# Kernel tuning notes

Hardware: AMD Instinct MI355X
Metric: run time of the kernel (lower is better)

The kernel has to match this reference:

```python
import jax, jax.numpy as jnp
import numpy as np

N_E = 8192
E_DIM = 256
N_TOK = 32768
MU = 0.25  # commitment weight; beta=0 so diversity loss is skipped


def setup_inputs() -> dict:
    key = jax.random.key(0)
    k1, k2, k3 = jax.random.split(key, 3)
    x = jax.random.normal(k1, (N_TOK, E_DIM), dtype=jnp.float32)
    # codebook init: uniform(-1/n_e, 1/n_e) as in the torch module
    emb = jax.random.uniform(k2, (N_E, E_DIM), dtype=jnp.float32,
                             minval=-1.0 / N_E, maxval=1.0 / N_E)
    label = jax.random.randint(k3, (N_TOK,), 0, 10, dtype=jnp.int32)
    return {"x": x, "emb": emb, "label": label, "idx": 0}


def reference(x, emb, label, idx):
    # latent: [N, e_dim]
    latent = x.reshape(-1, emb.shape[1])
    # pairwise squared distances via norm + matmul: [N, n_e]
    d = (jnp.sum(latent * latent, axis=1, keepdims=True)
         + jnp.sum(emb * emb, axis=1)[None, :]
         - 2.0 * (latent @ emb.T))
    indices = jnp.argmin(d, axis=-1)                 # [N]
    x_q = emb[indices].reshape(x.shape)              # gather
    commitment_loss = jnp.mean(jnp.square(jax.lax.stop_gradient(x_q) - x))
    codebook_loss = jnp.mean(jnp.square(x_q - jax.lax.stop_gradient(x)))
    loss = codebook_loss + MU * commitment_loss      # beta=0 -> no diversity term
    x_q_out = x + jax.lax.stop_gradient(x_q - x)     # straight-through estimator
    return x_q_out, loss, indices.reshape(x.shape[:-1])
```

## Files before the change

kernel.cpp:

```cpp
#include <hip/hip_runtime.h>
#include <float.h>
#include <stdint.h>

#define N_TOK 32768
#define N_E   8192
#define EDIM  256
#define MU_W  0.25f
#define NSPLIT 4
#define NRANGE 2048
#define BMr 128
#define BNr 256
#define NT8 8
#define TQ  4
#define MARGIN_F 4096.0f
#define OFFSETF (-0x1p21f)
#define XSCALE 512.0f
#define ESCALE -131072.0f

typedef _Float16 f16;
typedef _Float16 f16x8 __attribute__((ext_vector_type(8)));
typedef _Float16 f16x4 __attribute__((ext_vector_type(4)));
typedef float f32x4 __attribute__((ext_vector_type(4)));
typedef unsigned int u32;
typedef unsigned long long u64;

#define WS_EMB16   0
#define WS_SX      4194304
#define WS_SE      4325376
#define WS_SE25    4358144
#define WS_CAND    4390912
#define WS_PART    6488064
#define WS_RCNT    6619136
#define WS_RLIST   6619392
#define WS_RBEST   6750464

__device__ inline void gload_lds16(const void* g, void* l) {
  __builtin_amdgcn_global_load_lds(
      (const __attribute__((address_space(1))) unsigned int*)g,
      (__attribute__((address_space(3))) unsigned int*)l, 16, 0, 0);
}

__device__ inline u32 umax_(u32 a, u32 b) { return a > b ? a : b; }
__device__ inline u32 umin_(u32 a, u32 b) { return a < b ? a : b; }

__device__ inline u32 med3u(u32 a, u32 b, u32 c) {
  u32 r;
  asm("v_med3_u32 %0, %1, %2, %3" : "=v"(r) : "v"(a), "v"(b), "v"(c));
  return r;
}

__device__ inline void ins4max(u32 v, u32& a, u32& b, u32& c, u32& d) {
  u32 na = umax_(a, v);
  u32 nb = med3u(a, b, v);
  u32 nc = med3u(b, c, v);
  u32 nd = med3u(c, d, v);
  a = na; b = nb; c = nc; d = nd;
}

__global__ void zero_kernel(u32* p) { p[0] = 0u; }

__global__ __launch_bounds__(256) void conv_kernel(const float* __restrict__ src,
                                                   char* __restrict__ dst16,
                                                   float* __restrict__ norms,
                                                   float* __restrict__ norms25,
                                                   float scale, int write16, int nrows) {
  int wave = threadIdx.x >> 6;
  int lane = threadIdx.x & 63;
  int row = blockIdx.x * 4 + wave;
  if (row >= nrows) return;
  const float4 v = *(const float4*)(src + (size_t)row * EDIM + lane * 4);
  float s = (v.x * v.x + v.y * v.y) + (v.z * v.z + v.w * v.w);
#pragma unroll
  for (int off = 32; off >= 1; off >>= 1) s += __shfl_xor(s, off);
  if (lane == 0) {
    norms[row] = s;
    if (norms25) norms25[row] = s * 0x1p25f;
  }
  if (write16) {
    f16x4 h;
    h[0] = (f16)(v.x * scale); h[1] = (f16)(v.y * scale);
    h[2] = (f16)(v.z * scale); h[3] = (f16)(v.w * scale);
    int sw = (row & 7) << 4;
    *(f16x4*)(dst16 + (size_t)row * 512 + ((lane * 8) ^ sw)) = h;
  }
}

__global__ __launch_bounds__(512, 2) void vq_main(const float* __restrict__ x,
                                                  const char* __restrict__ e16,
                                                  const float* __restrict__ se25,
                                                  u32* __restrict__ cand) {
  __shared__ __align__(16) char Abuf[128 * 512];
  __shared__ __align__(16) char Bbuf[2][256 * 128];
  __shared__ u32 scratch[8][4][16][4];

  const int tid = threadIdx.x;
  const int lane = tid & 63;
  const int wid = tid >> 6;
  const int wm = wid >> 2;
  const int wn = wid & 3;
  const int l15 = lane & 15;
  const int lg  = lane >> 4;
  const int split = blockIdx.x & 3;
  const int bm = (blockIdx.x >> 2) * BMr;
  const int nbase = split * NRANGE;

  {
    const int row = tid >> 2, seg = tid & 3;
    const float4* xs = (const float4*)(x + (size_t)(bm + row) * EDIM + seg * 64);
    const int sw = (row & 7) << 4;
    char* ab = Abuf + row * 512;
#pragma unroll
    for (int u = 0; u < 8; ++u) {
      float4 a0 = xs[2 * u], a1 = xs[2 * u + 1];
      f16x8 hv;
      hv[0] = (f16)(a0.x * XSCALE); hv[1] = (f16)(a0.y * XSCALE);
      hv[2] = (f16)(a0.z * XSCALE); hv[3] = (f16)(a0.w * XSCALE);
      hv[4] = (f16)(a1.x * XSCALE); hv[5] = (f16)(a1.y * XSCALE);
      hv[6] = (f16)(a1.z * XSCALE); hv[7] = (f16)(a1.w * XSCALE);
      *(f16x8*)(ab + ((seg * 128 + u * 16) ^ sw)) = hv;
    }
  }
  {
    const char* src = e16 + (size_t)nbase * 512;
#pragma unroll
    for (int j = 0; j < 4; ++j) {
      int tt = j * 512 + tid;
      gload_lds16(src + (size_t)(tt >> 3) * 512 + (tt & 7) * 16, Bbuf[0] + tt * 16);
    }
  }
  __syncthreads();

  u32 d1[16], d2[16], d3[16], d4[16];
#pragma unroll
  for (int s = 0; s < 16; ++s) { d1[s] = 0u; d2[s] = 0u; d3[s] = 0u; d4[s] = 0u; }

  int cur = 0;
  for (int t = 0; t < NT8; ++t) {
    float sev[4];
#pragma unroll
    for (int ni = 0; ni < 4; ++ni)
      sev[ni] = se25[nbase + t * 256 + wn * 64 + ni * 16 + l15] + OFFSETF;

    f32x4 acc[4][4];
#pragma unroll
    for (int mi = 0; mi < 4; ++mi)
#pragma unroll
      for (int ni = 0; ni < 4; ++ni)
        acc[mi][ni] = (f32x4){sev[ni], sev[ni], sev[ni], sev[ni]};

    for (int q = 0; q < TQ; ++q) {
      const int step = t * TQ + q;
      if (step + 1 < NT8 * TQ) {
        const int t2 = (step + 1) >> 2, q2 = (step + 1) & 3;
        const char* src = e16 + (size_t)(nbase + t2 * 256) * 512 + q2 * 128;
        char* dst = Bbuf[cur ^ 1];
#pragma unroll
        for (int j = 0; j < 4; ++j) {
          int tt = j * 512 + tid;
          gload_lds16(src + (size_t)(tt >> 3) * 512 + (tt & 7) * 16, dst + tt * 16);
        }
      }
#pragma unroll
      for (int kk = 0; kk < 2; ++kk) {
        f16x8 av[4], bv[4];
#pragma unroll
        for (int mi = 0; mi < 4; ++mi) {
          const int ar = wm * 64 + mi * 16 + l15;
          av[mi] = *(const f16x8*)(Abuf + ar * 512 +
                                   ((q * 128 + kk * 64 + lg * 16) ^ ((ar & 7) << 4)));
        }
#pragma unroll
        for (int ni = 0; ni < 4; ++ni) {
          const int br = wn * 64 + ni * 16 + l15;
          bv[ni] = *(const f16x8*)(Bbuf[cur] + br * 128 +
                                   ((kk * 64 + lg * 16) ^ ((br & 7) << 4)));
        }
#pragma unroll
        for (int mi = 0; mi < 4; ++mi)
#pragma unroll
          for (int ni = 0; ni < 4; ++ni)
            acc[mi][ni] = __builtin_amdgcn_mfma_f32_16x16x32_f16(av[mi], bv[ni], acc[mi][ni], 0, 0, 0);
      }
      if (q == TQ - 1) {
#pragma unroll
        for (int ni = 0; ni < 4; ++ni) {
          const u32 id = (u32)((t << 8) | (wn << 6) | (ni << 4) | l15);
#pragma unroll
          for (int mi = 0; mi < 4; ++mi)
#pragma unroll
            for (int r = 0; r < 4; ++r) {
              u32 up = (__float_as_uint(acc[mi][ni][r]) & 0xFFFFF800u) | id;
              int s = mi * 4 + r;
              ins4max(up, d1[s], d2[s], d3[s], d4[s]);
            }
        }
      }
      __syncthreads();
      cur ^= 1;
    }
  }

#pragma unroll
  for (int off = 8; off >= 1; off >>= 1) {
#pragma unroll
    for (int s = 0; s < 16; ++s) {
      u32 e1 = (u32)__shfl_xor((int)d1[s], off);
      u32 e2 = (u32)__shfl_xor((int)d2[s], off);
      u32 e3 = (u32)__shfl_xor((int)d3[s], off);
      u32 e4 = (u32)__shfl_xor((int)d4[s], off);
      ins4max(e1, d1[s], d2[s], d3[s], d4[s]);
      ins4max(e2, d1[s], d2[s], d3[s], d4[s]);
      ins4max(e3, d1[s], d2[s], d3[s], d4[s]);
      ins4max(e4, d1[s], d2[s], d3[s], d4[s]);
    }
  }
  if (l15 == 0) {
#pragma unroll
    for (int s = 0; s < 16; ++s) {
      scratch[wid][lg][s][0] = d1[s];
      scratch[wid][lg][s][1] = d2[s];
      scratch[wid][lg][s][2] = d3[s];
      scratch[wid][lg][s][3] = d4[s];
    }
  }
  __syncthreads();
  if (tid < 128) {
    const int row = tid;
    const int wmr = row >> 6, mi = (row >> 4) & 3, lgr = (row >> 2) & 3, rr = row & 3;
    const int s = mi * 4 + rr;
    u32 a1 = scratch[wmr * 4][lgr][s][0];
    u32 a2 = scratch[wmr * 4][lgr][s][1];
    u32 a3 = scratch[wmr * 4][lgr][s][2];
    u32 a4 = scratch[wmr * 4][lgr][s][3];
#pragma unroll
    for (int w = 1; w < 4; ++w) {
#pragma unroll
      for (int c = 0; c < 4; ++c)
        ins4max(scratch[wmr * 4 + w][lgr][s][c], a1, a2, a3, a4);
    }
    size_t base = (size_t)split * (N_TOK * 4) + (size_t)(bm + row) * 4;
    cand[base + 0] = a1; cand[base + 1] = a2; cand[base + 2] = a3; cand[base + 3] = a4;
  }
}

__global__ __launch_bounds__(256) void vq_gather_kernel(
    const float* __restrict__ x, const float* __restrict__ emb,
    const float* __restrict__ sx, const float* __restrict__ se,
    const u32* __restrict__ cand,
    float* __restrict__ out_q, float* __restrict__ out_idx,
    float* __restrict__ partials,
    u32* __restrict__ rcnt, u32* __restrict__ rlist, u64* __restrict__ rbest) {
  const int token = blockIdx.x;
  const int tid = threadIdx.x;
  __shared__ int s_j;
  __shared__ int s_cnt;
  __shared__ int s_cj[16];
  __shared__ float s_dv[16];
  __shared__ float red[4];

  if (tid == 0) {
    u32 u[16];
    float uf[16];
    float gmin = FLT_MAX;
#pragma unroll
    for (int sp = 0; sp < 4; ++sp)
#pragma unroll
      for (int c = 0; c < 4; ++c) {
        u32 v = cand[(size_t)sp * (N_TOK * 4) + (size_t)token * 4 + c];
        u[sp * 4 + c] = v;
        float f = __uint_as_float(v);
        uf[sp * 4 + c] = f;
        gmin = fminf(gmin, f);
      }
    bool guard = false;
#pragma unroll
    for (int sp = 0; sp < 4; ++sp) guard = guard || (uf[sp * 4 + 3] <= gmin + MARGIN_F);
    int cnt;
    if (guard) {
      u32 slot = atomicAdd(rcnt, 1u);
      rlist[slot] = (u32)token;
      rbest[slot] = ~0ull;
      cnt = -1;
    } else {
      cnt = 0;
#pragma unroll
      for (int sp = 0; sp < 4; ++sp)
#pragma unroll
        for (int c = 0; c < 4; ++c) {
          int k = sp * 4 + c;
          if (uf[k] <= gmin + MARGIN_F)
            s_cj[cnt++] = sp * NRANGE + (int)(u[k] & 0x7FFu);
        }
      if (cnt == 1) s_j = s_cj[0];
    }
    s_cnt = cnt;
  }
  __syncthreads();
  int cnt = s_cnt;
  if (cnt < 0) return;
  if (cnt > 1 && tid < cnt) {
    int j = s_cj[tid];
    const float* xr = x + (size_t)token * EDIM;
    const float* er = emb + (size_t)j * EDIM;
    float a = 0.f;
    for (int k = 0; k < EDIM; ++k) a = fmaf(xr[k], er[k], a);
    s_dv[tid] = (sx[token] + se[j]) - 2.0f * a;
  }
  __syncthreads();
  if (cnt > 1 && tid == 0) {
    float bd = s_dv[0]; int bj = s_cj[0];
    for (int c = 1; c < cnt; ++c) {
      float d = s_dv[c]; int j = s_cj[c];
      if (d < bd || (d == bd && j < bj)) { bd = d; bj = j; }
    }
    s_j = bj;
  }
  __syncthreads();
  const int j = s_j;
  if (tid == 0) out_idx[token] = (float)j;
  float xv = x[(size_t)token * EDIM + tid];
  float q  = emb[(size_t)j * EDIM + tid];
  float diff = q - xv;
  out_q[(size_t)token * EDIM + tid] = xv + diff;
  float sq = diff * diff;
#pragma unroll
  for (int off = 32; off >= 1; off >>= 1) sq += __shfl_xor(sq, off);
  const int wave = tid >> 6, lane = tid & 63;
  if (lane == 0) red[wave] = sq;
  __syncthreads();
  if (tid == 0) partials[token] = (red[0] + red[1]) + (red[2] + red[3]);
}

__global__ __launch_bounds__(256) void vq_rescan_scan(
    const float* __restrict__ x, const float* __restrict__ emb,
    const float* __restrict__ sx, const float* __restrict__ se,
    const u32* __restrict__ rcnt, const u32* __restrict__ rlist,
    u64* __restrict__ rbest) {
  const int tid = threadIdx.x;
  const int n = (int)rcnt[0];
  const int total = n * 32;
  __shared__ float xs[EDIM];
  __shared__ u64 rw[4];

  for (int w = blockIdx.x; w < total; w += gridDim.x) {
    const int it = w >> 5, chunk = w & 31;
    const int token = (int)rlist[it];
    __syncthreads();
    xs[tid] = x[(size_t)token * EDIM + tid];
    __syncthreads();
    const float sxt = sx[token];
    const int j = chunk * 256 + tid;
    const float* er = emb + (size_t)j * EDIM;
    float a = 0.f;
#pragma unroll 8
    for (int k4 = 0; k4 < 64; ++k4) {
      float4 e4 = ((const float4*)er)[k4];
      float4 x4 = ((const float4*)xs)[k4];
      a = fmaf(x4.x, e4.x, a);
      a = fmaf(x4.y, e4.y, a);
      a = fmaf(x4.z, e4.z, a);
      a = fmaf(x4.w, e4.w, a);
    }
    float d = (sxt + se[j]) - 2.0f * a;
    u64 pk = ((u64)__float_as_uint(d) << 32) | (u32)j;
    const int lane = tid & 63, wave = tid >> 6;
#pragma unroll
    for (int off = 32; off >= 1; off >>= 1) {
      u64 o = __shfl_xor(pk, off);
      pk = o < pk ? o : pk;
    }
    if (lane == 0) rw[wave] = pk;
    __syncthreads();
    if (tid == 0) {
      u64 b = rw[0];
#pragma unroll
      for (int ww = 1; ww < 4; ++ww) b = rw[ww] < b ? rw[ww] : b;
      atomicMin(rbest + it, b);
    }
  }
}

__global__ __launch_bounds__(256) void vq_rescan_write(
    const float* __restrict__ x, const float* __restrict__ emb,
    const u32* __restrict__ rcnt, const u32* __restrict__ rlist,
    const u64* __restrict__ rbest,
    float* __restrict__ out_q, float* __restrict__ out_idx,
    float* __restrict__ partials) {
  const int tid = threadIdx.x;
  const int n = (int)rcnt[0];
  __shared__ float red[4];

  for (int it = blockIdx.x; it < n; it += gridDim.x) {
    const int token = (int)rlist[it];
    const int j = (int)(u32)(rbest[it] & 0xFFFFFFFFull);
    if (tid == 0) out_idx[token] = (float)j;
    float xv = x[(size_t)token * EDIM + tid];
    float q  = emb[(size_t)j * EDIM + tid];
    float diff = q - xv;
    out_q[(size_t)token * EDIM + tid] = xv + diff;
    float sq = diff * diff;
#pragma unroll
    for (int off = 32; off >= 1; off >>= 1) sq += __shfl_xor(sq, off);
    const int lane = tid & 63, wave = tid >> 6;
    __syncthreads();
    if (lane == 0) red[wave] = sq;
    __syncthreads();
    if (tid == 0) partials[token] = (red[0] + red[1]) + (red[2] + red[3]);
  }
}

__global__ __launch_bounds__(256) void vq_loss_kernel(const float* __restrict__ partials,
                                                      float* __restrict__ loss_out) {
  const int tid = threadIdx.x;
  float s = 0.f;
  for (int i = tid; i < N_TOK; i += 256) s += partials[i];
  __shared__ float red[4];
#pragma unroll
  for (int off = 32; off >= 1; off >>= 1) s += __shfl_xor(s, off);
  const int wave = tid >> 6, lane = tid & 63;
  if (lane == 0) red[wave] = s;
  __syncthreads();
  if (tid == 0) {
    float tot = (red[0] + red[1]) + (red[2] + red[3]);
    float mean = tot / (float)(N_TOK * EDIM);
    loss_out[0] = mean + MU_W * mean;
  }
}

extern "C" void kernel_launch(void* const* d_in, const int* in_sizes, int n_in,
                              void* d_out, int out_size, void* d_ws, size_t ws_size,
                              hipStream_t stream) {
  const float* x   = (const float*)d_in[0];
  const float* emb = (const float*)d_in[1];

  float* out      = (float*)d_out;
  float* out_q    = out;
  float* out_loss = out + (size_t)N_TOK * EDIM;
  float* out_idx  = out_loss + 1;

  char* w = (char*)d_ws;
  char*  emb16    = w + WS_EMB16;
  float* sx       = (float*)(w + WS_SX);
  float* se       = (float*)(w + WS_SE);
  float* se25     = (float*)(w + WS_SE25);
  u32*   cand     = (u32*)(w + WS_CAND);
  float* partials = (float*)(w + WS_PART);
  u32*   rcnt     = (u32*)(w + WS_RCNT);
  u32*   rlist    = (u32*)(w + WS_RLIST);
  u64*   rbest    = (u64*)(w + WS_RBEST);

  zero_kernel<<<1, 1, 0, stream>>>(rcnt);
  conv_kernel<<<N_E / 4, 256, 0, stream>>>(emb, emb16, se, se25, ESCALE, 1, N_E);
  conv_kernel<<<N_TOK / 4, 256, 0, stream>>>(x, nullptr, sx, nullptr, XSCALE, 0, N_TOK);

  vq_main<<<NSPLIT * (N_TOK / BMr), 512, 0, stream>>>(x, emb16, se25, cand);

  vq_gather_kernel<<<N_TOK, 256, 0, stream>>>(x, emb, sx, se, cand, out_q, out_idx, partials,
                                              rcnt, rlist, rbest);
  vq_rescan_scan<<<2048, 256, 0, stream>>>(x, emb, sx, se, rcnt, rlist, rbest);
  vq_rescan_write<<<64, 256, 0, stream>>>(x, emb, rcnt, rlist, rbest, out_q, out_idx, partials);
  vq_loss_kernel<<<1, 256, 0, stream>>>(partials, out_loss);
}
```

Baseline: 322.4 us.

## Retile fp16 codebook and activation layout into MFMA-fragment blocks, unroll q loop

Changes the global fp16 codebook layout and the shared-memory A/B layouts from XOR-swizzled row-major to a blocked 16-row fragment layout, so each lane's MFMA operand load is a contiguous 16-byte access at a precomputed offset. The inner q loop is fully unrolled with compile-time buffer selection, and the last prefetch wraps around instead of being branched out. This cuts address arithmetic and branching and aims for conflict-free LDS reads. The cost is a redundant final prefetch and a possible change in bank-conflict behaviour for the new layout.

```diff
diff --git a/kernel.cpp b/kernel.cpp
--- a/kernel.cpp
+++ b/kernel.cpp
@@ -9,9 +9,6 @@
 #define NSPLIT 4
 #define NRANGE 2048
 #define BMr 128
-#define BNr 256
-#define NT8 8
-#define TQ  4
 #define MARGIN_F 4096.0f
 #define OFFSETF (-0x1p21f)
 #define XSCALE 512.0f
@@ -80,8 +77,8 @@
     f16x4 h;
     h[0] = (f16)(v.x * scale); h[1] = (f16)(v.y * scale);
     h[2] = (f16)(v.z * scale); h[3] = (f16)(v.w * scale);
-    int sw = (row & 7) << 4;
-    *(f16x4*)(dst16 + (size_t)row * 512 + ((lane * 8) ^ sw)) = h;
+    *(f16x4*)(dst16 + (size_t)(row >> 4) * 8192 + (lane >> 1) * 256 +
+              (row & 15) * 16 + (lane & 1) * 8) = h;
   }
 }
 
@@ -90,7 +87,7 @@
                                                   const float* __restrict__ se25,
                                                   u32* __restrict__ cand) {
   __shared__ __align__(16) char Abuf[128 * 512];
-  __shared__ __align__(16) char Bbuf[2][256 * 128];
+  __shared__ __align__(16) char Bbuf[2 * 32768];
   __shared__ u32 scratch[8][4][16][4];
 
   const int tid = threadIdx.x;
@@ -104,11 +101,24 @@
   const int bm = (blockIdx.x >> 2) * BMr;
   const int nbase = split * NRANGE;
 
+  int aOff[4], bOff[4];
+#pragma unroll
+  for (int mi = 0; mi < 4; ++mi) aOff[mi] = (wm * 4 + mi) * 8192 + lg * 256 + l15 * 16;
+#pragma unroll
+  for (int ni = 0; ni < 4; ++ni) bOff[ni] = (wn * 4 + ni) * 2048 + lg * 256 + l15 * 16;
+
+  int svo[4], sdo[4];
+#pragma unroll
+  for (int j = 0; j < 4; ++j) {
+    int i = j * 512 + tid;
+    svo[j] = (i >> 7) * 8192 + (i & 127) * 16;
+    sdo[j] = i * 16;
+  }
+
   {
     const int row = tid >> 2, seg = tid & 3;
     const float4* xs = (const float4*)(x + (size_t)(bm + row) * EDIM + seg * 64);
-    const int sw = (row & 7) << 4;
-    char* ab = Abuf + row * 512;
+    const int abase = (row >> 4) * 8192 + (row & 15) * 16;
 #pragma unroll
     for (int u = 0; u < 8; ++u) {
       float4 a0 = xs[2 * u], a1 = xs[2 * u + 1];
@@ -117,16 +127,13 @@
       hv[2] = (f16)(a0.z * XSCALE); hv[3] = (f16)(a0.w * XSCALE);
       hv[4] = (f16)(a1.x * XSCALE); hv[5] = (f16)(a1.y * XSCALE);
       hv[6] = (f16)(a1.z * XSCALE); hv[7] = (f16)(a1.w * XSCALE);
-      *(f16x8*)(ab + ((seg * 128 + u * 16) ^ sw)) = hv;
+      *(f16x8*)&Abuf[abase + (seg * 8 + u) * 256] = hv;
     }
   }
   {
-    const char* src = e16 + (size_t)nbase * 512;
-#pragma unroll
-    for (int j = 0; j < 4; ++j) {
-      int tt = j * 512 + tid;
-      gload_lds16(src + (size_t)(tt >> 3) * 512 + (tt & 7) * 16, Bbuf[0] + tt * 16);
-    }
+    const size_t eb = ((size_t)(nbase >> 4)) * 8192;
+#pragma unroll
+    for (int j = 0; j < 4; ++j) gload_lds16(e16 + eb + svo[j], &Bbuf[sdo[j]]);
   }
   __syncthreads();
 
@@ -134,8 +141,9 @@
 #pragma unroll
   for (int s = 0; s < 16; ++s) { d1[s] = 0u; d2[s] = 0u; d3[s] = 0u; d4[s] = 0u; }
 
-  int cur = 0;
-  for (int t = 0; t < NT8; ++t) {
+  const int idl = wn * 64 + l15;
+
+  for (int t = 0; t < 8; ++t) {
     float sev[4];
 #pragma unroll
     for (int ni = 0; ni < 4; ++ni)
@@ -148,43 +156,36 @@
       for (int ni = 0; ni < 4; ++ni)
         acc[mi][ni] = (f32x4){sev[ni], sev[ni], sev[ni], sev[ni]};
 
-    for (int q = 0; q < TQ; ++q) {
-      const int step = t * TQ + q;
-      if (step + 1 < NT8 * TQ) {
-        const int t2 = (step + 1) >> 2, q2 = (step + 1) & 3;
-        const char* src = e16 + (size_t)(nbase + t2 * 256) * 512 + q2 * 128;
-        char* dst = Bbuf[cur ^ 1];
-#pragma unroll
-        for (int j = 0; j < 4; ++j) {
-          int tt = j * 512 + tid;
-          gload_lds16(src + (size_t)(tt >> 3) * 512 + (tt & 7) * 16, dst + tt * 16);
-        }
+#pragma unroll
+    for (int q = 0; q < 4; ++q) {
+      {
+        const int sn = (t * 4 + q + 1) & 31;
+        const int t2 = sn >> 2, q2 = sn & 3;
+        const size_t eb = ((size_t)(nbase >> 4) + t2 * 16) * 8192 + q2 * 2048;
+        const int db = ((q + 1) & 1) * 32768;
+#pragma unroll
+        for (int j = 0; j < 4; ++j) gload_lds16(e16 + eb + svo[j], &Bbuf[db + sdo[j]]);
       }
+      const int rb = (q & 1) * 32768;
 #pragma unroll
       for (int kk = 0; kk < 2; ++kk) {
         f16x8 av[4], bv[4];
 #pragma unroll
-        for (int mi = 0; mi < 4; ++mi) {
-          const int ar = wm * 64 + mi * 16 + l15;
-          av[mi] = *(const f16x8*)(Abuf + ar * 512 +
-                                   ((q * 128 + kk * 64 + lg * 16) ^ ((ar & 7) << 4)));
-        }
-#pragma unroll
-        for (int ni = 0; ni < 4; ++ni) {
-          const int br = wn * 64 + ni * 16 + l15;
-          bv[ni] = *(const f16x8*)(Bbuf[cur] + br * 128 +
-                                   ((kk * 64 + lg * 16) ^ ((br & 7) << 4)));
-        }
+        for (int mi = 0; mi < 4; ++mi)
+          av[mi] = *(const f16x8*)&Abuf[aOff[mi] + q * 2048 + kk * 1024];
+#pragma unroll
+        for (int ni = 0; ni < 4; ++ni)
+          bv[ni] = *(const f16x8*)&Bbuf[rb + bOff[ni] + kk * 1024];
 #pragma unroll
         for (int mi = 0; mi < 4; ++mi)
 #pragma unroll
           for (int ni = 0; ni < 4; ++ni)
             acc[mi][ni] = __builtin_amdgcn_mfma_f32_16x16x32_f16(av[mi], bv[ni], acc[mi][ni], 0, 0, 0);
       }
-      if (q == TQ - 1) {
+      if (q == 3) {
 #pragma unroll
         for (int ni = 0; ni < 4; ++ni) {
-          const u32 id = (u32)((t << 8) | (wn << 6) | (ni << 4) | l15);
+          const u32 id = (u32)(t * 256 + ni * 16 + idl);
 #pragma unroll
           for (int mi = 0; mi < 4; ++mi)
 #pragma unroll
@@ -196,7 +197,6 @@
         }
       }
       __syncthreads();
-      cur ^= 1;
     }
   }
 
```

Result: slower. 341.9 us (+6.0%).
